# Kernel tuning notes

Hardware: AMD Instinct MI355X
Metric: run time of the kernel (lower is better)

## Reference

```python
import jax, jax.numpy as jnp
import numpy as np

DIM = 1024
HID = 4096
E = 8
K = 3


def setup_inputs() -> dict:
    key = jax.random.key(0)
    ks = jax.random.split(key, 5)
    x = jax.random.normal(ks[0], (2, 2048, DIM), dtype=jnp.float32)
    # router: nn.Linear(dim, E) -- initialized to zero in source, but we use small
    # random weights so routing is non-degenerate for the correctness baseline.
    router_w = jax.random.normal(ks[1], (E, DIM), dtype=jnp.float32) * 0.02
    router_b = jax.random.normal(ks[2], (E,), dtype=jnp.float32) * 0.02
    # per-expert SwiGLU params: w12: [E, dim, 2*hid], w3: [E, hid, dim]
    w12 = jax.random.normal(ks[3], (E, DIM, 2 * HID), dtype=jnp.float32) * 0.02
    w3 = jax.random.normal(ks[4], (E, HID, DIM), dtype=jnp.float32) * 0.02
    return {"x": x, "router_w": router_w, "router_b": router_b, "w12": w12, "w3": w3}


def _moe(x, router_w, router_b, w12, w3):
    # router logits [B, S, E]
    logits = jnp.einsum("bsd,ed->bse", x, router_w) + router_b
    scores = jax.nn.sigmoid(logits)
    topk_scores, topk_idx = jax.lax.top_k(scores, K)  # [B,S,K]
    weights = topk_scores / (topk_scores.sum(axis=-1, keepdims=True) + 1e-6)
    # dense per-expert combine weight [B, S, E] (zero if expert not selected)
    onehot = jax.nn.one_hot(topk_idx, E, dtype=x.dtype)  # [B,S,K,E]
    dense_w = jnp.einsum("bske,bsk->bse", onehot, weights)
    out = jnp.zeros_like(x)
    for e in range(E):  # small fixed structural loop over experts
        x12 = x @ w12[e]  # [B,S,2H]
        x1, x2 = jnp.split(x12, 2, axis=-1)
        hidden = jax.nn.silu(x1) * x2
        out = out + (hidden @ w3[e]) * dense_w[..., e:e + 1]
    aux_loss = 0.01 * jnp.mean(logits ** 2)
    return out, aux_loss


def reference(x, router_w, router_b, w12, w3):
    return _moe(x, router_w, router_b, w12, w3)
```

## Files before the change

### kernel.cpp

```cpp
#include <hip/hip_runtime.h>
#include <math.h>

typedef unsigned short u16;
typedef __bf16 bf16x8 __attribute__((ext_vector_type(8)));
typedef float f32x4 __attribute__((ext_vector_type(4)));

#define T_TOK 4096
#define DIM   1024
#define HID   4096
#define NE    8
#define TOPK  3
#define NPAIR 12288

constexpr size_t OFF_CTRL = 0;
constexpr size_t OFF_XB   = 256;
constexpr size_t OFF_W12T = OFF_XB   + (size_t)T_TOK * DIM * 2;
constexpr size_t OFF_W3T  = OFF_W12T + (size_t)NE * 2 * HID * DIM * 2;
constexpr size_t OFF_HID  = OFF_W3T  + (size_t)NE * DIM * HID * 2;
constexpr size_t OFF_Y    = OFF_HID  + (size_t)NPAIR * HID * 2;
constexpr size_t OFF_PTOK = OFF_Y    + (size_t)NPAIR * DIM * 4;
constexpr size_t OFF_TE   = OFF_PTOK + (size_t)NPAIR * 4;
constexpr size_t OFF_TW   = OFF_TE   + (size_t)T_TOK * TOPK * 4;
constexpr size_t OFF_TS   = OFF_TW   + (size_t)T_TOK * TOPK * 4;

__device__ __forceinline__ u16 f2bf(float f) {
    unsigned u = __builtin_bit_cast(unsigned, f);
    u += 0x7fffu + ((u >> 16) & 1u);
    return (u16)(u >> 16);
}

__device__ __forceinline__ void ld_g2l(const u16* g, u16* l) {
    __builtin_amdgcn_global_load_lds((__attribute__((address_space(1))) unsigned*)(g),
                                     (__attribute__((address_space(3))) unsigned*)(l),
                                     16, 0, 0);
}

#define VMCNT(N) asm volatile("s_waitcnt vmcnt(" #N ")" ::: "memory")
#define LGKM0  asm volatile("s_waitcnt lgkmcnt(0)" ::: "memory")
#define SBAR   __builtin_amdgcn_s_barrier()
#define SCHED0 __builtin_amdgcn_sched_barrier(0)
#define PRIO1  __builtin_amdgcn_s_setprio(1)
#define PRIO0  __builtin_amdgcn_s_setprio(0)

#define STAGE_A02(dst) { ld_g2l(srcA[0], (dst) + (0 * 64 + wave * 8) * 64); \
                         ld_g2l(srcA[2], (dst) + (2 * 64 + wave * 8) * 64); }
#define STAGE_B01(dst) { ld_g2l(srcB[0], (dst) + 16384 + (0 * 64 + wave * 8) * 64); \
                         ld_g2l(srcB[1], (dst) + 16384 + (1 * 64 + wave * 8) * 64); }
#define STAGE_B23(dst) { ld_g2l(srcB[2], (dst) + 16384 + (2 * 64 + wave * 8) * 64); \
                         ld_g2l(srcB[3], (dst) + 16384 + (3 * 64 + wave * 8) * 64); }
#define STAGE_A13(dst) { ld_g2l(srcA[1], (dst) + (1 * 64 + wave * 8) * 64); \
                         ld_g2l(srcA[3], (dst) + (3 * 64 + wave * 8) * 64); }
#define ADV()          { _Pragma("unroll") \
                         for (int r_ = 0; r_ < 4; ++r_) { srcA[r_] += 64; srcB[r_] += 64; } }

__global__ __launch_bounds__(256) void transpose_cast_kernel(const float* __restrict__ in,
                                                             u16* __restrict__ out, int K, int N) {
    __shared__ float tile[64][33];
    const float* inp = in + (size_t)blockIdx.z * K * N;
    u16* outp = out + (size_t)blockIdx.z * K * N;
    const int n0 = blockIdx.x * 32, k0 = blockIdx.y * 64;
    const int tid = threadIdx.x;
#pragma unroll
    for (int i = 0; i < 2; ++i) {
        int k = i * 32 + (tid >> 3);
        int c4 = (tid & 7) * 4;
        float4 f = *(const float4*)(inp + (size_t)(k0 + k) * N + n0 + c4);
        tile[k][c4 + 0] = f.x; tile[k][c4 + 1] = f.y;
        tile[k][c4 + 2] = f.z; tile[k][c4 + 3] = f.w;
    }
    __syncthreads();
    const int n = tid >> 3, c = (tid & 7) * 8;
    u16 buf[8];
#pragma unroll
    for (int j = 0; j < 8; ++j) buf[j] = f2bf(tile[c + j][n]);
    *(uint4*)(outp + (size_t)(n0 + n) * K + k0 + c) = *(uint4*)buf;
}

__global__ __launch_bounds__(256) void router_kernel(const float* __restrict__ x,
                                                     const float* __restrict__ rw,
                                                     const float* __restrict__ rb,
                                                     u16* __restrict__ xb,
                                                     int* __restrict__ tok_expert,
                                                     float* __restrict__ tok_w,
                                                     int* __restrict__ ctrl,
                                                     float* __restrict__ aux) {
    __shared__ int hist[NE];
    __shared__ float auxsh;
    const int tid = threadIdx.x;
    if (tid < NE) hist[tid] = 0;
    if (tid == NE) auxsh = 0.f;
    __syncthreads();

    const int wave = tid >> 6, lane = tid & 63;
    const int t = blockIdx.x * 4 + wave;
    const float* xr = x + (size_t)t * DIM;
    u16* xbr = xb + (size_t)t * DIM;

    float p[NE];
#pragma unroll
    for (int e = 0; e < NE; e++) p[e] = 0.f;
#pragma unroll
    for (int q = 0; q < 4; ++q) {
        const int d = q * 256 + lane * 4;
        float4 f = *(const float4*)(xr + d);
        uint2 v;
        v.x = (unsigned)f2bf(f.x) | ((unsigned)f2bf(f.y) << 16);
        v.y = (unsigned)f2bf(f.z) | ((unsigned)f2bf(f.w) << 16);
        *(uint2*)(xbr + d) = v;
#pragma unroll
        for (int e = 0; e < NE; e++) {
            float4 w = *(const float4*)(rw + e * DIM + d);
            p[e] += f.x * w.x + f.y * w.y + f.z * w.z + f.w * w.w;
        }
    }
#pragma unroll
    for (int e = 0; e < NE; e++) {
#pragma unroll
        for (int off = 32; off; off >>= 1) p[e] += __shfl_down(p[e], off, 64);
    }
    if (lane == 0) {
        float s[NE]; float auxs = 0.f;
#pragma unroll
        for (int e = 0; e < NE; e++) {
            float lg = p[e] + rb[e];
            auxs += lg * lg;
            s[e] = 1.f / (1.f + __expf(-lg));
        }
        atomicAdd(&auxsh, auxs);
        unsigned mask = 0; float wsum = 0.f;
        int idxs[TOPK]; float vals[TOPK];
        for (int k = 0; k < TOPK; k++) {
            float best = -1.f; int bi = 0;
            for (int e = 0; e < NE; e++)
                if (!((mask >> e) & 1u) && s[e] > best) { best = s[e]; bi = e; }
            mask |= 1u << bi; idxs[k] = bi; vals[k] = best; wsum += best;
        }
        wsum += 1e-6f;
        for (int k = 0; k < TOPK; k++) {
            tok_expert[t * TOPK + k] = idxs[k];
            tok_w[t * TOPK + k] = vals[k] / wsum;
            atomicAdd(&hist[idxs[k]], 1);
        }
    }
    __syncthreads();
    if (tid < NE) { int h = hist[tid]; if (h) atomicAdd(&ctrl[tid], h); }
    if (tid == NE) atomicAdd(aux, auxsh * (0.01f / 32768.0f));
}

__global__ void scan_kernel(int* __restrict__ ctrl) {
    if (threadIdx.x == 0) {
        int acc = 0;
        for (int e = 0; e < NE; e++) { ctrl[8 + e] = acc; acc += ctrl[e]; }
    }
}

__global__ __launch_bounds__(256) void assign_kernel(const int* __restrict__ tok_expert,
                                                     const float* __restrict__ tok_w,
                                                     int* __restrict__ ctrl,
                                                     int* __restrict__ pair_token,
                                                     int* __restrict__ tok_slot) {
    int t = blockIdx.x * blockDim.x + threadIdx.x;
    if (t >= T_TOK) return;
    for (int k = 0; k < TOPK; k++) {
        int e = tok_expert[t * TOPK + k];
        int pos = atomicAdd(&ctrl[16 + e], 1);
        int slot = ctrl[8 + e] + pos;
        pair_token[slot] = t;
        tok_slot[t * TOPK + k] = slot;
    }
}

__global__ __launch_bounds__(512, 2) void gemm1_kernel(const u16* __restrict__ xb,
                                                       const u16* __restrict__ w12t,
                                                       const int* __restrict__ pair_token,
                                                       const int* __restrict__ ctrl,
                                                       u16* __restrict__ hidden) {
    const int e = blockIdx.z;
    const int cnt = ctrl[e];
    if ((int)blockIdx.y * 256 >= cnt) return;
    const int off = ctrl[8 + e];
    const int rowbase = off + blockIdx.y * 256;
    const int rowend = off + cnt;
    const int n0 = blockIdx.x * 128;

    extern __shared__ __align__(16) u16 lds[];

    const int tid = threadIdx.x;
    const int wave = tid >> 6, lane = tid & 63;
    const int srow = tid >> 3;
    const int scol = ((tid & 7) ^ (srow & 7)) * 8;

    const u16* srcA[4];
    const u16* srcB[4];
#pragma unroll
    for (int r = 0; r < 4; ++r) {
        int sr = rowbase + r * 64 + srow;
        int tok = (sr < rowend) ? pair_token[sr] : 0;
        srcA[r] = xb + (size_t)tok * DIM + scol;
    }
#pragma unroll
    for (int r = 0; r < 2; ++r) {
        srcB[r]     = w12t + ((size_t)e * 2 * HID + n0 + r * 64 + srow) * DIM + scol;
        srcB[r + 2] = srcB[r] + (size_t)HID * DIM;
    }

    const int wm = wave >> 2, wn = wave & 3;
    const int lrow = lane & 15, lq = lane >> 4, xm = lrow & 7;
    const int so0 = ((lq ^ xm) << 3);
    const int so1 = (((4 | lq) ^ xm) << 3);

    f32x4 acc0[8][2], acc1[8][2];
#pragma unroll
    for (int mf = 0; mf < 8; ++mf)
#pragma unroll
        for (int nf = 0; nf < 2; ++nf) { acc0[mf][nf] = (f32x4)0.f; acc1[mf][nf] = (f32x4)0.f; }

    STAGE_A02(lds); STAGE_B01(lds);
    STAGE_B23(lds);
    STAGE_A13(lds);
    ADV();

    const int NT = DIM / 64;
    for (int kt = 0; kt < NT; ++kt) {
        u16* cur = lds + (kt & 1) * 32768;
        u16* nxt = lds + ((kt & 1) ^ 1) * 32768;
        const u16* sA = cur;
        const u16* sB = cur + 16384;
        const bool notlast = (kt < NT - 1);

        bf16x8 a[4][2], b0[2][2], b1[2][2];
        VMCNT(4); SBAR; SCHED0;
#pragma unroll
        for (int mf = 0; mf < 4; ++mf) {
            const u16* base = sA + (wm * 128 + mf * 16 + lrow) * 64;
            a[mf][0] = *(const bf16x8*)(base + so0);
            a[mf][1] = *(const bf16x8*)(base + so1);
        }
#pragma unroll
        for (int nf = 0; nf < 2; ++nf) {
            const u16* base = sB + (wn * 32 + nf * 16 + lrow) * 64;
            b0[nf][0] = *(const bf16x8*)(base + so0);
            b0[nf][1] = *(const bf16x8*)(base + so1);
        }
        if (notlast) { STAGE_A02(nxt); STAGE_B01(nxt); }
        LGKM0; SCHED0;
        PRIO1;
#pragma unroll
        for (int mf = 0; mf < 4; ++mf)
#pragma unroll
            for (int nf = 0; nf < 2; ++nf) {
                acc0[mf][nf] = __builtin_amdgcn_mfma_f32_16x16x32_bf16(a[mf][0], b0[nf][0], acc0[mf][nf], 0, 0, 0);
                acc0[mf][nf] = __builtin_amdgcn_mfma_f32_16x16x32_bf16(a[mf][1], b0[nf][1], acc0[mf][nf], 0, 0, 0);
            }
        PRIO0;
        if (notlast) { VMCNT(6); } else { VMCNT(2); }
        SBAR; SCHED0;
#pragma unroll
        for (int nf = 0; nf < 2; ++nf) {
            const u16* base = sB + 128 * 64 + (wn * 32 + nf * 16 + lrow) * 64;
            b1[nf][0] = *(const bf16x8*)(base + so0);
            b1[nf][1] = *(const bf16x8*)(base + so1);
        }
        if (notlast) STAGE_B23(nxt);
        LGKM0; SCHED0;
        PRIO1;
#pragma unroll
        for (int mf = 0; mf < 4; ++mf)
#pragma unroll
            for (int nf = 0; nf < 2; ++nf) {
                acc1[mf][nf] = __builtin_amdgcn_mfma_f32_16x16x32_bf16(a[mf][0], b1[nf][0], acc1[mf][nf], 0, 0, 0);
                acc1[mf][nf] = __builtin_amdgcn_mfma_f32_16x16x32_bf16(a[mf][1], b1[nf][1], acc1[mf][nf], 0, 0, 0);
            }
        PRIO0;
        if (notlast) { VMCNT(6); } else { VMCNT(0); }
        SBAR; SCHED0;
#pragma unroll
        for (int mf = 0; mf < 4; ++mf) {
            const u16* base = sA + (wm * 128 + (mf + 4) * 16 + lrow) * 64;
            a[mf][0] = *(const bf16x8*)(base + so0);
            a[mf][1] = *(const bf16x8*)(base + so1);
        }
        if (notlast) { STAGE_A13(nxt); ADV(); }
        LGKM0; SCHED0;
        PRIO1;
#pragma unroll
        for (int mf = 0; mf < 4; ++mf)
#pragma unroll
            for (int nf = 0; nf < 2; ++nf) {
                acc1[mf + 4][nf] = __builtin_amdgcn_mfma_f32_16x16x32_bf16(a[mf][0], b1[nf][0], acc1[mf + 4][nf], 0, 0, 0);
                acc1[mf + 4][nf] = __builtin_amdgcn_mfma_f32_16x16x32_bf16(a[mf][1], b1[nf][1], acc1[mf + 4][nf], 0, 0, 0);
            }
        PRIO0;
        SBAR;
        PRIO1;
#pragma unroll
        for (int mf = 0; mf < 4; ++mf)
#pragma unroll
            for (int nf = 0; nf < 2; ++nf) {
                acc0[mf + 4][nf] = __builtin_amdgcn_mfma_f32_16x16x32_bf16(a[mf][0], b0[nf][0], acc0[mf + 4][nf], 0, 0, 0);
                acc0[mf + 4][nf] = __builtin_amdgcn_mfma_f32_16x16x32_bf16(a[mf][1], b0[nf][1], acc0[mf + 4][nf], 0, 0, 0);
            }
        PRIO0;
    }

#pragma unroll
    for (int mf = 0; mf < 8; ++mf) {
        const int gr0 = rowbase + wm * 128 + mf * 16 + lq * 4;
#pragma unroll
        for (int nf = 0; nf < 2; ++nf) {
            const int gc = n0 + wn * 32 + nf * 16 + lrow;
#pragma unroll
            for (int r = 0; r < 4; ++r) {
                const int gr = gr0 + r;
                if (gr < rowend) {
                    float x1 = acc0[mf][nf][r], x2 = acc1[mf][nf][r];
                    float h = x1 / (1.f + __expf(-x1)) * x2;
                    hidden[(size_t)gr * HID + gc] = f2bf(h);
                }
            }
        }
    }
}

__global__ __launch_bounds__(512, 2) void gemm2_kernel(const u16* __restrict__ hidden,
                                                       const u16* __restrict__ w3t,
                                                       const int* __restrict__ ctrl,
                                                       float* __restrict__ ybuf) {
    const int e = blockIdx.z;
    const int cnt = ctrl[e];
    if ((int)blockIdx.y * 256 >= cnt) return;
    const int off = ctrl[8 + e];
    const int rowbase = off + blockIdx.y * 256;
    const int rowend = off + cnt;
    const int n0 = blockIdx.x * 256;

    extern __shared__ __align__(16) u16 lds[];

    const int tid = threadIdx.x;
    const int wave = tid >> 6, lane = tid & 63;
    const int srow = tid >> 3;
    const int scol = ((tid & 7) ^ (srow & 7)) * 8;

    const u16* srcA[4];
    const u16* srcB[4];
#pragma unroll
    for (int r = 0; r < 4; ++r) {
        int sr = rowbase + r * 64 + srow;
        if (sr > NPAIR - 1) sr = NPAIR - 1;
        srcA[r] = hidden + (size_t)sr * HID + scol;
        srcB[r] = w3t + ((size_t)e * DIM + n0 + r * 64 + srow) * HID + scol;
    }

    const int wm = wave >> 2, wn = wave & 3;
    const int lrow = lane & 15, lq = lane >> 4, xm = lrow & 7;
    const int so0 = ((lq ^ xm) << 3);
    const int so1 = (((4 | lq) ^ xm) << 3);

    f32x4 acc[8][4];
#pragma unroll
    for (int mf = 0; mf < 8; ++mf)
#pragma unroll
        for (int nf = 0; nf < 4; ++nf) acc[mf][nf] = (f32x4)0.f;

    STAGE_A02(lds); STAGE_B01(lds);
    STAGE_B23(lds);
    STAGE_A13(lds);
    ADV();

    const int NT = HID / 64;
    for (int kt = 0; kt < NT; ++kt) {
        u16* cur = lds + (kt & 1) * 32768;
        u16* nxt = lds + ((kt & 1) ^ 1) * 32768;
        const u16* sA = cur;
        const u16* sB = cur + 16384;
        const bool notlast = (kt < NT - 1);

        bf16x8 a[4][2], b[4][2];
        VMCNT(4); SBAR; SCHED0;
#pragma unroll
        for (int mf = 0; mf < 4; ++mf) {
            const u16* base = sA + (wm * 128 + mf * 16 + lrow) * 64;
            a[mf][0] = *(const bf16x8*)(base + so0);
            a[mf][1] = *(const bf16x8*)(base + so1);
        }
#pragma unroll
        for (int nf = 0; nf < 2; ++nf) {
            const u16* base = sB + (nf * 64 + wn * 16 + lrow) * 64;
            b[nf][0] = *(const bf16x8*)(base + so0);
            b[nf][1] = *(const bf16x8*)(base + so1);
        }
        if (notlast) { STAGE_A02(nxt); STAGE_B01(nxt); }
        LGKM0; SCHED0;
        PRIO1;
#pragma unroll
        for (int mf = 0; mf < 4; ++mf)
#pragma unroll
            for (int nf = 0; nf < 2; ++nf) {
                acc[mf][nf] = __builtin_amdgcn_mfma_f32_16x16x32_bf16(a[mf][0], b[nf][0], acc[mf][nf], 0, 0, 0);
                acc[mf][nf] = __builtin_amdgcn_mfma_f32_16x16x32_bf16(a[mf][1], b[nf][1], acc[mf][nf], 0, 0, 0);
            }
        PRIO0;
        if (notlast) { VMCNT(6); } else { VMCNT(2); }
        SBAR; SCHED0;
#pragma unroll
        for (int nf = 2; nf < 4; ++nf) {
            const u16* base = sB + (nf * 64 + wn * 16 + lrow) * 64;
            b[nf][0] = *(const bf16x8*)(base + so0);
            b[nf][1] = *(const bf16x8*)(base + so1);
        }
        if (notlast) STAGE_B23(nxt);
        LGKM0; SCHED0;
        PRIO1;
#pragma unroll
        for (int mf = 0; mf < 4; ++mf)
#pragma unroll
            for (int nf = 2; nf < 4; ++nf) {
                acc[mf][nf] = __builtin_amdgcn_mfma_f32_16x16x32_bf16(a[mf][0], b[nf][0], acc[mf][nf], 0, 0, 0);
                acc[mf][nf] = __builtin_amdgcn_mfma_f32_16x16x32_bf16(a[mf][1], b[nf][1], acc[mf][nf], 0, 0, 0);
            }
        PRIO0;
        if (notlast) { VMCNT(6); } else { VMCNT(0); }
        SBAR; SCHED0;
#pragma unroll
        for (int mf = 0; mf < 4; ++mf) {
            const u16* base = sA + (wm * 128 + (mf + 4) * 16 + lrow) * 64;
            a[mf][0] = *(const bf16x8*)(base + so0);
            a[mf][1] = *(const bf16x8*)(base + so1);
        }
        if (notlast) { STAGE_A13(nxt); ADV(); }
        LGKM0; SCHED0;
        PRIO1;
#pragma unroll
        for (int mf = 0; mf < 4; ++mf)
#pragma unroll
            for (int nf = 2; nf < 4; ++nf) {
                acc[mf + 4][nf] = __builtin_amdgcn_mfma_f32_16x16x32_bf16(a[mf][0], b[nf][0], acc[mf + 4][nf], 0, 0, 0);
                acc[mf + 4][nf] = __builtin_amdgcn_mfma_f32_16x16x32_bf16(a[mf][1], b[nf][1], acc[mf + 4][nf], 0, 0, 0);
            }
        PRIO0;
        SBAR;
        PRIO1;
#pragma unroll
        for (int mf = 0; mf < 4; ++mf)
#pragma unroll
            for (int nf = 0; nf < 2; ++nf) {
                acc[mf + 4][nf] = __builtin_amdgcn_mfma_f32_16x16x32_bf16(a[mf][0], b[nf][0], acc[mf + 4][nf], 0, 0, 0);
                acc[mf + 4][nf] = __builtin_amdgcn_mfma_f32_16x16x32_bf16(a[mf][1], b[nf][1], acc[mf + 4][nf], 0, 0, 0);
            }
        PRIO0;
    }

#pragma unroll
    for (int mf = 0; mf < 8; ++mf) {
        const int gr0 = rowbase + wm * 128 + mf * 16 + lq * 4;
#pragma unroll
        for (int nf = 0; nf < 4; ++nf) {
            const int gc = n0 + nf * 64 + wn * 16 + lrow;
#pragma unroll
            for (int r = 0; r < 4; ++r) {
                const int gr = gr0 + r;
                if (gr < rowend) ybuf[(size_t)gr * DIM + gc] = acc[mf][nf][r];
            }
        }
    }
}

__global__ __launch_bounds__(256) void combine_kernel(const float* __restrict__ ybuf,
                                                      const int* __restrict__ tok_slot,
                                                      const float* __restrict__ tok_w,
                                                      float* __restrict__ out) {
    const int t = blockIdx.x;
    const int d = threadIdx.x * 4;
    const int s0 = tok_slot[t * 3 + 0], s1 = tok_slot[t * 3 + 1], s2 = tok_slot[t * 3 + 2];
    const float w0 = tok_w[t * 3 + 0], w1 = tok_w[t * 3 + 1], w2 = tok_w[t * 3 + 2];
    const float4 a0 = *(const float4*)(ybuf + (size_t)s0 * DIM + d);
    const float4 a1 = *(const float4*)(ybuf + (size_t)s1 * DIM + d);
    const float4 a2 = *(const float4*)(ybuf + (size_t)s2 * DIM + d);
    float4 o;
    o.x = w0 * a0.x + w1 * a1.x + w2 * a2.x;
    o.y = w0 * a0.y + w1 * a1.y + w2 * a2.y;
    o.z = w0 * a0.z + w1 * a1.z + w2 * a2.z;
    o.w = w0 * a0.w + w1 * a1.w + w2 * a2.w;
    *(float4*)(out + (size_t)t * DIM + d) = o;
}

extern "C" void kernel_launch(void* const* d_in, const int* in_sizes, int n_in,
                              void* d_out, int out_size, void* d_ws, size_t ws_size,
                              hipStream_t stream) {
    const float* x   = (const float*)d_in[0];
    const float* rw  = (const float*)d_in[1];
    const float* rb  = (const float*)d_in[2];
    const float* w12 = (const float*)d_in[3];
    const float* w3  = (const float*)d_in[4];
    float* out = (float*)d_out;
    char* ws = (char*)d_ws;

    int*   ctrl       = (int*)(ws + OFF_CTRL);
    u16*   xb         = (u16*)(ws + OFF_XB);
    u16*   w12t       = (u16*)(ws + OFF_W12T);
    u16*   w3t        = (u16*)(ws + OFF_W3T);
    u16*   hidden     = (u16*)(ws + OFF_HID);
    float* ybuf       = (float*)(ws + OFF_Y);
    int*   pair_token = (int*)(ws + OFF_PTOK);
    int*   tok_expert = (int*)(ws + OFF_TE);
    float* tok_w      = (float*)(ws + OFF_TW);
    int*   tok_slot   = (int*)(ws + OFF_TS);

    static bool attr_set = false;
    if (!attr_set) {
        hipFuncSetAttribute((const void*)gemm1_kernel, hipFuncAttributeMaxDynamicSharedMemorySize, 131072);
        hipFuncSetAttribute((const void*)gemm2_kernel, hipFuncAttributeMaxDynamicSharedMemorySize, 131072);
        attr_set = true;
    }

    hipMemsetAsync(ctrl, 0, 256, stream);
    hipMemsetAsync(out + (size_t)T_TOK * DIM, 0, sizeof(float), stream);

    router_kernel<<<T_TOK / 4, 256, 0, stream>>>(x, rw, rb, xb, tok_expert, tok_w, ctrl,
                                                 out + (size_t)T_TOK * DIM);
    transpose_cast_kernel<<<dim3(2 * HID / 32, DIM / 64, NE), 256, 0, stream>>>(w12, w12t, DIM, 2 * HID);
    transpose_cast_kernel<<<dim3(DIM / 32, HID / 64, NE), 256, 0, stream>>>(w3, w3t, HID, DIM);
    scan_kernel<<<1, 64, 0, stream>>>(ctrl);
    assign_kernel<<<16, 256, 0, stream>>>(tok_expert, tok_w, ctrl, pair_token, tok_slot);

    gemm1_kernel<<<dim3(HID / 128, 16, NE), 512, 131072, stream>>>(xb, w12t, pair_token, ctrl, hidden);
    gemm2_kernel<<<dim3(DIM / 256, 16, NE), 512, 131072, stream>>>(hidden, w3t, ctrl, ybuf);
    combine_kernel<<<T_TOK, 256, 0, stream>>>(ybuf, tok_slot, tok_w, out);
    (void)in_sizes; (void)n_in; (void)out_size; (void)ws_size;
}
```

Before: 894.5 us.

## Restructure GEMM main-loop pipeline with fewer prefetch phases and extra barriers

Both expert GEMM kernels (gate/up with SwiGLU, and down projection) now issue the B23 and A13 prefetch stages together in the third phase instead of splitting them across phases. The vmcnt waits are retuned to match, one mid-iteration wait-plus-barrier pair is removed, and extra workgroup barriers and scheduling fences are placed before each MFMA block. The aim is to keep the 8-wave workgroup in lockstep and cluster the global-to-LDS loads so MFMA issue is less disturbed. The extra barriers add synchronization cost, and bunching the loads may expose more memory latency.

```diff
diff --git a/kernel.cpp b/kernel.cpp
--- a/kernel.cpp
+++ b/kernel.cpp
@@ -216,8 +216,7 @@
         for (int nf = 0; nf < 2; ++nf) { acc0[mf][nf] = (f32x4)0.f; acc1[mf][nf] = (f32x4)0.f; }
 
     STAGE_A02(lds); STAGE_B01(lds);
-    STAGE_B23(lds);
-    STAGE_A13(lds);
+    STAGE_B23(lds); STAGE_A13(lds);
     ADV();
 
     const int NT = DIM / 64;
@@ -243,7 +242,7 @@
             b0[nf][1] = *(const bf16x8*)(base + so1);
         }
         if (notlast) { STAGE_A02(nxt); STAGE_B01(nxt); }
-        LGKM0; SCHED0;
+        SCHED0; SBAR; LGKM0; SCHED0;
         PRIO1;
 #pragma unroll
         for (int mf = 0; mf < 4; ++mf)
@@ -252,8 +251,8 @@
                 acc0[mf][nf] = __builtin_amdgcn_mfma_f32_16x16x32_bf16(a[mf][0], b0[nf][0], acc0[mf][nf], 0, 0, 0);
                 acc0[mf][nf] = __builtin_amdgcn_mfma_f32_16x16x32_bf16(a[mf][1], b0[nf][1], acc0[mf][nf], 0, 0, 0);
             }
-        PRIO0;
-        if (notlast) { VMCNT(6); } else { VMCNT(2); }
+        PRIO0; SCHED0;
+        if (notlast) { VMCNT(4); } else { VMCNT(0); }
         SBAR; SCHED0;
 #pragma unroll
         for (int nf = 0; nf < 2; ++nf) {
@@ -261,8 +260,7 @@
             b1[nf][0] = *(const bf16x8*)(base + so0);
             b1[nf][1] = *(const bf16x8*)(base + so1);
         }
-        if (notlast) STAGE_B23(nxt);
-        LGKM0; SCHED0;
+        SCHED0; SBAR; LGKM0; SCHED0;
         PRIO1;
 #pragma unroll
         for (int mf = 0; mf < 4; ++mf)
@@ -271,17 +269,15 @@
                 acc1[mf][nf] = __builtin_amdgcn_mfma_f32_16x16x32_bf16(a[mf][0], b1[nf][0], acc1[mf][nf], 0, 0, 0);
                 acc1[mf][nf] = __builtin_amdgcn_mfma_f32_16x16x32_bf16(a[mf][1], b1[nf][1], acc1[mf][nf], 0, 0, 0);
             }
-        PRIO0;
-        if (notlast) { VMCNT(6); } else { VMCNT(0); }
-        SBAR; SCHED0;
+        PRIO0; SCHED0;
 #pragma unroll
         for (int mf = 0; mf < 4; ++mf) {
             const u16* base = sA + (wm * 128 + (mf + 4) * 16 + lrow) * 64;
             a[mf][0] = *(const bf16x8*)(base + so0);
             a[mf][1] = *(const bf16x8*)(base + so1);
         }
-        if (notlast) { STAGE_A13(nxt); ADV(); }
-        LGKM0; SCHED0;
+        if (notlast) { STAGE_B23(nxt); STAGE_A13(nxt); ADV(); }
+        SCHED0; SBAR; LGKM0; SCHED0;
         PRIO1;
 #pragma unroll
         for (int mf = 0; mf < 4; ++mf)
@@ -290,7 +286,7 @@
                 acc1[mf + 4][nf] = __builtin_amdgcn_mfma_f32_16x16x32_bf16(a[mf][0], b1[nf][0], acc1[mf + 4][nf], 0, 0, 0);
                 acc1[mf + 4][nf] = __builtin_amdgcn_mfma_f32_16x16x32_bf16(a[mf][1], b1[nf][1], acc1[mf + 4][nf], 0, 0, 0);
             }
-        PRIO0;
+        PRIO0; SCHED0;
         SBAR;
         PRIO1;
 #pragma unroll
@@ -300,7 +296,7 @@
                 acc0[mf + 4][nf] = __builtin_amdgcn_mfma_f32_16x16x32_bf16(a[mf][0], b0[nf][0], acc0[mf + 4][nf], 0, 0, 0);
                 acc0[mf + 4][nf] = __builtin_amdgcn_mfma_f32_16x16x32_bf16(a[mf][1], b0[nf][1], acc0[mf + 4][nf], 0, 0, 0);
             }
-        PRIO0;
+        PRIO0; SCHED0;
     }
 
 #pragma unroll
@@ -363,8 +359,7 @@
         for (int nf = 0; nf < 4; ++nf) acc[mf][nf] = (f32x4)0.f;
 
     STAGE_A02(lds); STAGE_B01(lds);
-    STAGE_B23(lds);
-    STAGE_A13(lds);
+    STAGE_B23(lds); STAGE_A13(lds);
     ADV();
 
     const int NT = HID / 64;
@@ -390,7 +385,7 @@
             b[nf][1] = *(const bf16x8*)(base + so1);
         }
         if (notlast) { STAGE_A02(nxt); STAGE_B01(nxt); }
-        LGKM0; SCHED0;
+        SCHED0; SBAR; LGKM0; SCHED0;
         PRIO1;
 #pragma unroll
         for (int mf = 0; mf < 4; ++mf)
@@ -399,8 +394,8 @@
                 acc[mf][nf] = __builtin_amdgcn_mfma_f32_16x16x32_bf16(a[mf][0], b[nf][0], acc[mf][nf], 0, 0, 0);
                 acc[mf][nf] = __builtin_amdgcn_mfma_f32_16x16x32_bf16(a[mf][1], b[nf][1], acc[mf][nf], 0, 0, 0);
             }
-        PRIO0;
-        if (notlast) { VMCNT(6); } else { VMCNT(2); }
+        PRIO0; SCHED0;
+        if (notlast) { VMCNT(4); } else { VMCNT(0); }
         SBAR; SCHED0;
 #pragma unroll
         for (int nf = 2; nf < 4; ++nf) {
@@ -408,8 +403,7 @@
             b[nf][0] = *(const bf16x8*)(base + so0);
             b[nf][1] = *(const bf16x8*)(base + so1);
         }
-        if (notlast) STAGE_B23(nxt);
-        LGKM0; SCHED0;
+        SCHED0; SBAR; LGKM0; SCHED0;
         PRIO1;
 #pragma unroll
         for (int mf = 0; mf < 4; ++mf)
@@ -418,17 +412,15 @@
                 acc[mf][nf] = __builtin_amdgcn_mfma_f32_16x16x32_bf16(a[mf][0], b[nf][0], acc[mf][nf], 0, 0, 0);
                 acc[mf][nf] = __builtin_amdgcn_mfma_f32_16x16x32_bf16(a[mf][1], b[nf][1], acc[mf][nf], 0, 0, 0);
             }
-        PRIO0;
-        if (notlast) { VMCNT(6); } else { VMCNT(0); }
-        SBAR; SCHED0;
+        PRIO0; SCHED0;
 #pragma unroll
         for (int mf = 0; mf < 4; ++mf) {
             const u16* base = sA + (wm * 128 + (mf + 4) * 16 + lrow) * 64;
             a[mf][0] = *(const bf16x8*)(base + so0);
             a[mf][1] = *(const bf16x8*)(base + so1);
         }
-        if (notlast) { STAGE_A13(nxt); ADV(); }
-        LGKM0; SCHED0;
+        if (notlast) { STAGE_B23(nxt); STAGE_A13(nxt); ADV(); }
+        SCHED0; SBAR; LGKM0; SCHED0;
         PRIO1;
 #pragma unroll
         for (int mf = 0; mf < 4; ++mf)
@@ -437,7 +429,7 @@
                 acc[mf + 4][nf] = __builtin_amdgcn_mfma_f32_16x16x32_bf16(a[mf][0], b[nf][0], acc[mf + 4][nf], 0, 0, 0);
                 acc[mf + 4][nf] = __builtin_amdgcn_mfma_f32_16x16x32_bf16(a[mf][1], b[nf][1], acc[mf + 4][nf], 0, 0, 0);
             }
-        PRIO0;
+        PRIO0; SCHED0;
         SBAR;
         PRIO1;
 #pragma unroll
@@ -447,7 +439,7 @@
                 acc[mf + 4][nf] = __builtin_amdgcn_mfma_f32_16x16x32_bf16(a[mf][0], b[nf][0], acc[mf + 4][nf], 0, 0, 0);
                 acc[mf + 4][nf] = __builtin_amdgcn_mfma_f32_16x16x32_bf16(a[mf][1], b[nf][1], acc[mf + 4][nf], 0, 0, 0);
             }
-        PRIO0;
+        PRIO0; SCHED0;
     }
 
 #pragma unroll
```

Measured after the change: 906.6 us. No clear change (+1.4%).
